# Kernel tuning notes

Measured on AMD Instinct MI355X. Metric: run time of the kernel, lower is better.

The kernel has to match this reference:

```python
import jax, jax.numpy as jnp
import numpy as np

B, S, E, H = 4, 2048, 2048, 1  # batch, seq, n_embd, n_head (source only runs with H=1)
LN_EPS = 1e-5


def _layernorm(x, g, b):
    m = jnp.mean(x, axis=-1, keepdims=True)
    v = jnp.mean(jnp.square(x - m), axis=-1, keepdims=True)
    return (x - m) * jax.lax.rsqrt(v + LN_EPS) * g + b


def setup_inputs() -> dict:
    key = jax.random.key(0)
    ks = jax.random.split(key, 8)
    sc = 0.02
    return {
        "x": jax.random.normal(ks[0], (B, S, E), jnp.float32),
        "mask": jnp.ones((B, S, 1, 1), jnp.int32),
        # attention params (torch Linear stored transposed: (in, out))
        "w_attn": jax.random.normal(ks[1], (E, H * E), jnp.float32) * sc,
        "b_attn": jnp.zeros((H * E,), jnp.float32),
        "w_kv": jax.random.normal(ks[2], (E, H * E), jnp.float32) * sc,
        "b_kv": jnp.zeros((H * E,), jnp.float32),
        "ln1_g": jnp.ones((E,), jnp.float32),
        "ln1_b": jnp.zeros((E,), jnp.float32),
        # MLP params
        "w_fc": jax.random.normal(ks[3], (E, 4 * E), jnp.float32) * sc,
        "b_fc": jnp.zeros((4 * E,), jnp.float32),
        "w_mproj": jax.random.normal(ks[4], (4 * E, E), jnp.float32) * sc,
        "b_mproj": jnp.zeros((E,), jnp.float32),
        "ln2_g": jnp.ones((E,), jnp.float32),
        "ln2_b": jnp.zeros((E,), jnp.float32),
    }


def reference(x, mask, w_attn, b_attn, w_kv, b_kv, ln1_g, ln1_b,
              w_fc, b_fc, w_mproj, b_mproj, ln2_g, ln2_b):
    # ---- Attention (faithful to source: einsum binds 'h' to the seq axis) ----
    h_attn = (x @ w_attn + b_attn).reshape(B, S, H, E)  # (b, s, h, d)
    h_proj = (x @ w_kv + b_kv).reshape(B, S, H, E)      # (b, s, h, d)
    # score[b, s, m, l] = sum_d h_attn[b, s, l, d] * h_proj[b, s, m, d]
    attn_score = jnp.einsum('bhld,bhmd->bhml', h_attn, h_proj)  # (B, S, H, H)
    attn_score = jnp.where(mask == 0, jnp.float32(-1e9), attn_score)
    attn_prob = jax.nn.softmax(attn_score, axis=-1)
    attn_vec = jnp.einsum('bhml,bhmd->bhld', attn_prob, h_proj)  # (B, S, H, E)
    attn_out = attn_vec.reshape(B, S, H * E)
    # (dropouts are identity in eval mode)
    # ---- Residual + LN + MLP + Residual + LN ----
    h = _layernorm(x + attn_out, ln1_g, ln1_b)
    h_mlp = jax.nn.gelu(h @ w_fc + b_fc, approximate=False)
    h_mlp = h_mlp @ w_mproj + b_mproj
    return _layernorm(h_mlp + x, ln2_g, ln2_b)
```

## Files before the change

kernel.cpp:

```cpp
#include <hip/hip_runtime.h>
#include <hip/hip_bf16.h>
#include <stdint.h>


typedef __attribute__((ext_vector_type(4))) float f32x4;
typedef __attribute__((ext_vector_type(8))) __bf16 bf16x8;
typedef __attribute__((ext_vector_type(8))) unsigned short ushort8;

__device__ __forceinline__ unsigned short f2bf(float f) {
  unsigned int u = __float_as_uint(f);
  return (unsigned short)((u + 0x7FFFu + ((u >> 16) & 1u)) >> 16);
}

__device__ __forceinline__ void gload_lds16(const void* g, void* l) {
  __builtin_amdgcn_global_load_lds(
      (const __attribute__((address_space(1))) unsigned int*)(uintptr_t)g,
      (__attribute__((address_space(3))) unsigned int*)(unsigned int)(uintptr_t)l,
      16, 0, 0);
}

#define WAITLGK(n) asm volatile("s_waitcnt lgkmcnt(" #n ")" ::: "memory")
#define WAITVM(n) asm volatile("s_waitcnt vmcnt(" #n ")" ::: "memory")
#define SBAR() __builtin_amdgcn_s_barrier()
#define SCHED0() __builtin_amdgcn_sched_barrier(0)

__global__ __launch_bounds__(256) void cvt_bf16_kernel(
    const float* __restrict__ in, unsigned short* __restrict__ out, int n8) {
  int i = blockIdx.x * 256 + threadIdx.x;
  if (i >= n8) return;
  const size_t base = (size_t)i * 8;
  float4 a = *(const float4*)(in + base);
  float4 b = *(const float4*)(in + base + 4);
  ushort8 o;
  o[0] = f2bf(a.x); o[1] = f2bf(a.y); o[2] = f2bf(a.z); o[3] = f2bf(a.w);
  o[4] = f2bf(b.x); o[5] = f2bf(b.y); o[6] = f2bf(b.z); o[7] = f2bf(b.w);
  *(ushort8*)(out + base) = o;
}

__global__ __launch_bounds__(256) void transpose_cvt(
    const float* __restrict__ W, unsigned short* __restrict__ WT, int R, int C) {
  __shared__ unsigned short t[64][66];
  const int c0 = blockIdx.x * 64, r0 = blockIdx.y * 64;
  const int tid = threadIdx.x;
  const int lr = tid >> 4;
  const int lc = (tid & 15) * 4;
#pragma unroll
  for (int p = 0; p < 4; ++p) {
    const int r = lr + p * 16;
    float4 v = *(const float4*)(W + (size_t)(r0 + r) * C + c0 + lc);
    t[r][lc + 0] = f2bf(v.x);
    t[r][lc + 1] = f2bf(v.y);
    t[r][lc + 2] = f2bf(v.z);
    t[r][lc + 3] = f2bf(v.w);
  }
  __syncthreads();
#pragma unroll
  for (int p = 0; p < 4; ++p) {
    const int oc = lr + p * 16;
    ushort4 o;
    o.x = t[lc + 0][oc];
    o.y = t[lc + 1][oc];
    o.z = t[lc + 2][oc];
    o.w = t[lc + 3][oc];
    *(ushort4*)(WT + (size_t)(c0 + oc) * R + r0 + lc) = o;
  }
}

template <int EPI>
__global__ __launch_bounds__(512, 2) void gemm256(
    const unsigned short* __restrict__ A, const unsigned short* __restrict__ BT,
    const float* __restrict__ bias, const float* __restrict__ xres,
    void* __restrict__ out, int N, int K) {
  __shared__ unsigned short lds[2][2][256 * 64];

  const int tid = threadIdx.x;
  const int lane = tid & 63;
  const int w = tid >> 6;
  const int wm = w >> 2;
  const int wn = w & 3;

  const int nbn = N / 256;
  const int nwg = gridDim.x;
  const int bid = blockIdx.x;
  const int wg = (bid & 7) * (nwg >> 3) + (bid >> 3);
  const int bm = wg / nbn, bn = wg % nbn;

  const int nt = K / 64;

  const int srow = w * 8 + (lane >> 3);
  const int schunk = (lane & 7) ^ ((lane >> 3) & 7);
  const unsigned short* gA = A + (size_t)(bm * 256 + srow) * K + schunk * 8;
  const unsigned short* gB = BT + (size_t)(bn * 256 + srow) * K + schunk * 8;

  auto STAGE = [&](int buf, int op, int half, int tile) {
    const int tc = tile < nt ? tile : nt - 1;
    const unsigned short* g =
        (op ? gB : gA) + (size_t)(half * 128) * K + (size_t)tc * 64;
    unsigned short* l = &lds[buf][op][(half * 128 + w * 8) * 64];
    gload_lds16(g, l);
    gload_lds16(g + (size_t)64 * K, l + 64 * 64);
  };

  const int rA = wm * 128 + (lane & 15);
  const int rB = wn * 64 + (lane & 15);
  const int kq = lane >> 4;
  const int x7 = lane & 7;
  const int c0 = ((kq ^ x7) << 4);
  const int c1 = (((4 + kq) ^ x7) << 4);

  f32x4 acc[8][4] = {};
  bf16x8 aS0[4][2], aS1[4][2], b0v[2][2], b1v[2][2];

#define READ_ALO(buf)                                              \
  {                                                                \
    const char* p = (const char*)&lds[buf][0][0] + rA * 128;       \
    _Pragma("unroll") for (int mf = 0; mf < 4; ++mf) {             \
      aS0[mf][0] = *(const bf16x8*)(p + mf * 2048 + c0);           \
      aS0[mf][1] = *(const bf16x8*)(p + mf * 2048 + c1);           \
    }                                                              \
  }
#define READ_AHI(buf)                                              \
  {                                                                \
    const char* p = (const char*)&lds[buf][0][0] + rA * 128 + 8192;\
    _Pragma("unroll") for (int mf = 0; mf < 4; ++mf) {             \
      aS1[mf][0] = *(const bf16x8*)(p + mf * 2048 + c0);           \
      aS1[mf][1] = *(const bf16x8*)(p + mf * 2048 + c1);           \
    }                                                              \
  }
#define READ_B0(buf)                                               \
  {                                                                \
    const char* p = (const char*)&lds[buf][1][0] + rB * 128;       \
    _Pragma("unroll") for (int nf = 0; nf < 2; ++nf) {             \
      b0v[nf][0] = *(const bf16x8*)(p + nf * 2048 + c0);           \
      b0v[nf][1] = *(const bf16x8*)(p + nf * 2048 + c1);           \
    }                                                              \
  }
#define READ_B1(buf)                                               \
  {                                                                \
    const char* p = (const char*)&lds[buf][1][0] + rB * 128 + 4096;\
    _Pragma("unroll") for (int nf = 0; nf < 2; ++nf) {             \
      b1v[nf][0] = *(const bf16x8*)(p + nf * 2048 + c0);           \
      b1v[nf][1] = *(const bf16x8*)(p + nf * 2048 + c1);           \
    }                                                              \
  }
#define CLUSTER(ASET, BSET, MO, NO)                                         \
  __builtin_amdgcn_s_setprio(1);                                            \
  _Pragma("unroll") for (int mf = 0; mf < 4; ++mf)                          \
      _Pragma("unroll") for (int nf = 0; nf < 2; ++nf)                      \
          _Pragma("unroll") for (int ks = 0; ks < 2; ++ks)                  \
              acc[MO + mf][NO + nf] =                                       \
                  __builtin_amdgcn_mfma_f32_16x16x32_bf16(                  \
                      ASET[mf][ks], BSET[nf][ks], acc[MO + mf][NO + nf],    \
                      0, 0, 0);                                             \
  __builtin_amdgcn_s_setprio(0);

  STAGE(0, 0, 0, 0); STAGE(0, 0, 1, 0); STAGE(0, 1, 0, 0); STAGE(0, 1, 1, 0);
  STAGE(1, 0, 0, 1); STAGE(1, 0, 1, 1); STAGE(1, 1, 0, 1); STAGE(1, 1, 1, 1);
  WAITVM(8);
  SBAR();
  READ_ALO(0);
  READ_B0(0);

  for (int t = 0; t < nt; ++t) {
    const int cb = t & 1, ob = cb ^ 1;
    READ_B1(cb);
    WAITLGK(4);
    SCHED0();
    CLUSTER(aS0, b0v, 0, 0);
    SBAR();
    READ_AHI(cb);
    WAITLGK(8);
    SCHED0();
    CLUSTER(aS0, b1v, 0, 2);
    SBAR();
    STAGE(cb, 0, 0, t + 2);
    WAITLGK(0);
    SCHED0();
    CLUSTER(aS1, b0v, 4, 0);
    WAITVM(2);
    SBAR();
    READ_ALO(ob);
    READ_B0(ob);
    STAGE(cb, 0, 1, t + 2);
    STAGE(cb, 1, 0, t + 2);
    STAGE(cb, 1, 1, t + 2);
    WAITLGK(12);
    SCHED0();
    CLUSTER(aS1, b1v, 4, 2);
    SBAR();
  }
  WAITVM(0);

  const int col0 = bn * 256 + wn * 64 + (lane & 15);
  const int row0 = bm * 256 + wm * 128 + ((lane >> 4) << 2);
  float bv[4];
#pragma unroll
  for (int n = 0; n < 4; ++n) bv[n] = bias[col0 + n * 16];
#pragma unroll
  for (int mf = 0; mf < 8; ++mf) {
#pragma unroll
    for (int j = 0; j < 4; ++j) {
      const size_t row = (size_t)(row0 + mf * 16 + j);
#pragma unroll
      for (int n = 0; n < 4; ++n) {
        const size_t idx = row * N + col0 + n * 16;
        float v = acc[mf][n][j] + bv[n];
        if (EPI == 0) {
          ((float*)out)[idx] = v + xres[idx];
        } else {
          float ge = 0.5f * v * (1.0f + erff(v * 0.7071067811865475f));
          ((unsigned short*)out)[idx] = f2bf(ge);
        }
      }
    }
  }
#undef READ_ALO
#undef READ_AHI
#undef READ_B0
#undef READ_B1
#undef CLUSTER
}

template <int OUT_BF16>
__global__ __launch_bounds__(256) void ln_row(const float* __restrict__ tin,
                                              const float* __restrict__ gw,
                                              const float* __restrict__ bw,
                                              void* __restrict__ outp) {
  const int row = blockIdx.x;
  const int tid = threadIdx.x;
  const size_t base = (size_t)row * 2048 + tid * 8;
  alignas(16) float v[8];
  *(float4*)(v) = *(const float4*)(tin + base);
  *(float4*)(v + 4) = *(const float4*)(tin + base + 4);
  float s = 0.f, q = 0.f;
#pragma unroll
  for (int i = 0; i < 8; ++i) { s += v[i]; q += v[i] * v[i]; }
#pragma unroll
  for (int m = 32; m >= 1; m >>= 1) {
    s += __shfl_xor(s, m);
    q += __shfl_xor(q, m);
  }
  __shared__ float red[8];
  if ((tid & 63) == 0) {
    red[tid >> 6] = s;
    red[4 + (tid >> 6)] = q;
  }
  __syncthreads();
  s = red[0] + red[1] + red[2] + red[3];
  q = red[4] + red[5] + red[6] + red[7];
  const float mean = s * (1.0f / 2048.0f);
  float var = q * (1.0f / 2048.0f) - mean * mean;
  var = fmaxf(var, 0.0f);
  const float rstd = rsqrtf(var + 1e-5f);
  alignas(16) float gv[8], bv[8];
  *(float4*)(gv) = *(const float4*)(gw + (size_t)tid * 8);
  *(float4*)(gv + 4) = *(const float4*)(gw + (size_t)tid * 8 + 4);
  *(float4*)(bv) = *(const float4*)(bw + (size_t)tid * 8);
  *(float4*)(bv + 4) = *(const float4*)(bw + (size_t)tid * 8 + 4);
  if (OUT_BF16) {
    ushort8 o;
#pragma unroll
    for (int i = 0; i < 8; ++i)
      o[i] = f2bf((v[i] - mean) * rstd * gv[i] + bv[i]);
    *(ushort8*)((unsigned short*)outp + base) = o;
  } else {
    alignas(16) float r[8];
#pragma unroll
    for (int i = 0; i < 8; ++i) r[i] = (v[i] - mean) * rstd * gv[i] + bv[i];
    *(float4*)((float*)outp + base) = *(float4*)(r);
    *(float4*)((float*)outp + base + 4) = *(float4*)(r + 4);
  }
}

extern "C" void kernel_launch(void* const* d_in, const int* in_sizes, int n_in,
                              void* d_out, int out_size, void* d_ws,
                              size_t ws_size, hipStream_t stream) {
  constexpr int M = 8192;
  constexpr int E = 2048;
  constexpr int F = 8192;
  const size_t MiB = 1ull << 20;

  const float* x = (const float*)d_in[0];
  const float* w_kv = (const float*)d_in[4];
  const float* b_kv = (const float*)d_in[5];
  const float* ln1_g = (const float*)d_in[6];
  const float* ln1_b = (const float*)d_in[7];
  const float* w_fc = (const float*)d_in[8];
  const float* b_fc = (const float*)d_in[9];
  const float* w_mproj = (const float*)d_in[10];
  const float* b_mproj = (const float*)d_in[11];
  const float* ln2_g = (const float*)d_in[12];
  const float* ln2_b = (const float*)d_in[13];
  float* out = (float*)d_out;
  char* ws = (char*)d_ws;

  float* tbuf = out;

  int nch;
  unsigned short *xb, *wkvT, *wfcT, *wmpT, *hb, *gch;
  if (ws_size >= 224 * MiB) {
    nch = 1;
    gch = (unsigned short*)(ws + 0);
    xb = (unsigned short*)(ws + 0);
    wkvT = (unsigned short*)(ws + 32 * MiB);
    wfcT = (unsigned short*)(ws + 128 * MiB);
    wmpT = (unsigned short*)(ws + 160 * MiB);
    hb = (unsigned short*)(ws + 192 * MiB);
  } else if (ws_size >= 160 * MiB) {
    nch = 2;
    gch = (unsigned short*)(ws + 0);
    xb = (unsigned short*)(ws + 0);
    wkvT = (unsigned short*)(ws + 32 * MiB);
    hb = (unsigned short*)(ws + 64 * MiB);
    wfcT = (unsigned short*)(ws + 96 * MiB);
    wmpT = (unsigned short*)(ws + 128 * MiB);
  } else {
    nch = 4;
    gch = (unsigned short*)(ws + 0);
    xb = (unsigned short*)(ws + 0);
    wkvT = (unsigned short*)(ws + 32 * MiB);
    hb = (unsigned short*)(ws + 32 * MiB);
    wfcT = (unsigned short*)(ws + 64 * MiB);
    wmpT = (unsigned short*)(ws + 96 * MiB);
  }

  cvt_bf16_kernel<<<(M * E / 8 + 255) / 256, 256, 0, stream>>>(x, xb, M * E / 8);
  transpose_cvt<<<dim3(E / 64, E / 64), 256, 0, stream>>>(w_kv, wkvT, E, E);
  transpose_cvt<<<dim3(F / 64, E / 64), 256, 0, stream>>>(w_fc, wfcT, E, F);
  transpose_cvt<<<dim3(E / 64, F / 64), 256, 0, stream>>>(w_mproj, wmpT, F, E);

  gemm256<0><<<(M / 256) * (E / 256), 512, 0, stream>>>(xb, wkvT, b_kv, x,
                                                        tbuf, E, E);
  ln_row<1><<<M, 256, 0, stream>>>(tbuf, ln1_g, ln1_b, hb);
  const int Mc = M / nch;
  for (int c = 0; c < nch; ++c) {
    const size_t roff = (size_t)c * Mc;
    gemm256<1><<<(Mc / 256) * (F / 256), 512, 0, stream>>>(
        hb + roff * E, wfcT, b_fc, nullptr, gch, F, E);
    gemm256<0><<<(Mc / 256) * (E / 256), 512, 0, stream>>>(
        gch, wmpT, b_mproj, x + roff * E, tbuf + roff * E, E, F);
  }
  ln_row<0><<<M, 256, 0, stream>>>(tbuf, ln2_g, ln2_b, out);
}
```

Measured before the change: 689.7 us.

## Restructure GEMM LDS layout into quarter tiles with finer-grained 8-wave staging schedule

Reorganizes the GEMM shared-memory buffer into per-half sub-tiles so each staged chunk matches one MFMA cluster's operands. The main loop is unrolled by two tiles, and global-to-LDS loads are interleaved at quarter granularity between MFMA clusters with explicit vmcnt/lgkmcnt waits and barriers. Only one A fragment set stays in registers, which lowers register pressure. The aim is to overlap loads with compute more evenly, at the cost of more barriers per tile and a riskier hand-written dependency schedule.

```diff
diff --git a/kernel.cpp b/kernel.cpp
--- a/kernel.cpp
+++ b/kernel.cpp
@@ -22,7 +22,6 @@
 #define WAITLGK(n) asm volatile("s_waitcnt lgkmcnt(" #n ")" ::: "memory")
 #define WAITVM(n) asm volatile("s_waitcnt vmcnt(" #n ")" ::: "memory")
 #define SBAR() __builtin_amdgcn_s_barrier()
-#define SCHED0() __builtin_amdgcn_sched_barrier(0)
 
 __global__ __launch_bounds__(256) void cvt_bf16_kernel(
     const float* __restrict__ in, unsigned short* __restrict__ out, int n8) {
@@ -71,13 +70,14 @@
     const unsigned short* __restrict__ A, const unsigned short* __restrict__ BT,
     const float* __restrict__ bias, const float* __restrict__ xres,
     void* __restrict__ out, int N, int K) {
-  __shared__ unsigned short lds[2][2][256 * 64];
+  __shared__ unsigned short L[2][2][2][8192];
 
   const int tid = threadIdx.x;
   const int lane = tid & 63;
   const int w = tid >> 6;
   const int wm = w >> 2;
   const int wn = w & 3;
+  const int l15 = lane & 15;
 
   const int nbn = N / 256;
   const int nwg = gridDim.x;
@@ -89,109 +89,123 @@
 
   const int srow = w * 8 + (lane >> 3);
   const int schunk = (lane & 7) ^ ((lane >> 3) & 7);
-  const unsigned short* gA = A + (size_t)(bm * 256 + srow) * K + schunk * 8;
-  const unsigned short* gB = BT + (size_t)(bn * 256 + srow) * K + schunk * 8;
-
-  auto STAGE = [&](int buf, int op, int half, int tile) {
-    const int tc = tile < nt ? tile : nt - 1;
-    const unsigned short* g =
-        (op ? gB : gA) + (size_t)(half * 128) * K + (size_t)tc * 64;
-    unsigned short* l = &lds[buf][op][(half * 128 + w * 8) * 64];
-    gload_lds16(g, l);
-    gload_lds16(g + (size_t)64 * K, l + 64 * 64);
-  };
-
-  const int rA = wm * 128 + (lane & 15);
-  const int rB = wn * 64 + (lane & 15);
+  const unsigned short* pb[2][2][2];
+#pragma unroll
+  for (int h = 0; h < 2; ++h)
+#pragma unroll
+    for (int j = 0; j < 2; ++j) {
+      pb[0][h][j] =
+          A + (size_t)(bm * 256 + j * 128 + h * 64 + srow) * K + schunk * 8;
+      pb[1][h][j] = BT +
+                    (size_t)(bn * 256 + ((srow >> 5) + 2 * j) * 64 + h * 32 +
+                             (srow & 31)) * K +
+                    schunk * 8;
+    }
+
+#define STAGE(BUF, OP, H, TILE)                                            \
+  {                                                                        \
+    const size_t ko_ = (size_t)(TILE) * 64;                                \
+    gload_lds16(pb[OP][H][0] + ko_, &L[BUF][OP][H][w * 512]);              \
+    gload_lds16(pb[OP][H][1] + ko_, &L[BUF][OP][H][w * 512 + 4096]);       \
+  }
+
   const int kq = lane >> 4;
   const int x7 = lane & 7;
-  const int c0 = ((kq ^ x7) << 4);
-  const int c1 = (((4 + kq) ^ x7) << 4);
+  const int cc0 = ((kq ^ x7) << 4);
+  const int cc1 = (((4 + kq) ^ x7) << 4);
+  const int rAoff = (wm * 64 + l15) * 128;
+  const int rBoff = (wn * 32 + l15) * 128;
 
   f32x4 acc[8][4] = {};
-  bf16x8 aS0[4][2], aS1[4][2], b0v[2][2], b1v[2][2];
-
-#define READ_ALO(buf)                                              \
-  {                                                                \
-    const char* p = (const char*)&lds[buf][0][0] + rA * 128;       \
-    _Pragma("unroll") for (int mf = 0; mf < 4; ++mf) {             \
-      aS0[mf][0] = *(const bf16x8*)(p + mf * 2048 + c0);           \
-      aS0[mf][1] = *(const bf16x8*)(p + mf * 2048 + c1);           \
-    }                                                              \
-  }
-#define READ_AHI(buf)                                              \
-  {                                                                \
-    const char* p = (const char*)&lds[buf][0][0] + rA * 128 + 8192;\
-    _Pragma("unroll") for (int mf = 0; mf < 4; ++mf) {             \
-      aS1[mf][0] = *(const bf16x8*)(p + mf * 2048 + c0);           \
-      aS1[mf][1] = *(const bf16x8*)(p + mf * 2048 + c1);           \
-    }                                                              \
-  }
-#define READ_B0(buf)                                               \
-  {                                                                \
-    const char* p = (const char*)&lds[buf][1][0] + rB * 128;       \
-    _Pragma("unroll") for (int nf = 0; nf < 2; ++nf) {             \
-      b0v[nf][0] = *(const bf16x8*)(p + nf * 2048 + c0);           \
-      b0v[nf][1] = *(const bf16x8*)(p + nf * 2048 + c1);           \
-    }                                                              \
-  }
-#define READ_B1(buf)                                               \
-  {                                                                \
-    const char* p = (const char*)&lds[buf][1][0] + rB * 128 + 4096;\
-    _Pragma("unroll") for (int nf = 0; nf < 2; ++nf) {             \
-      b1v[nf][0] = *(const bf16x8*)(p + nf * 2048 + c0);           \
-      b1v[nf][1] = *(const bf16x8*)(p + nf * 2048 + c1);           \
-    }                                                              \
-  }
-#define CLUSTER(ASET, BSET, MO, NO)                                         \
+  bf16x8 aF[4][2], b0F[2][2], b1F[2][2];
+
+#define RD_A(BUF, H)                                                   \
+  {                                                                    \
+    const char* p_ = (const char*)&L[BUF][0][H][0] + rAoff;            \
+    _Pragma("unroll") for (int mf = 0; mf < 4; ++mf) {                 \
+      aF[mf][0] = *(const bf16x8*)(p_ + mf * 2048 + cc0);              \
+      aF[mf][1] = *(const bf16x8*)(p_ + mf * 2048 + cc1);              \
+    }                                                                  \
+  }
+#define RD_B(BUF, H, DST)                                              \
+  {                                                                    \
+    const char* p_ = (const char*)&L[BUF][1][H][0] + rBoff;            \
+    _Pragma("unroll") for (int nf = 0; nf < 2; ++nf) {                 \
+      DST[nf][0] = *(const bf16x8*)(p_ + nf * 2048 + cc0);             \
+      DST[nf][1] = *(const bf16x8*)(p_ + nf * 2048 + cc1);             \
+    }                                                                  \
+  }
+#define CLUSTER(BSET, MO, NO)                                               \
   __builtin_amdgcn_s_setprio(1);                                            \
   _Pragma("unroll") for (int mf = 0; mf < 4; ++mf)                          \
       _Pragma("unroll") for (int nf = 0; nf < 2; ++nf)                      \
           _Pragma("unroll") for (int ks = 0; ks < 2; ++ks)                  \
               acc[MO + mf][NO + nf] =                                       \
                   __builtin_amdgcn_mfma_f32_16x16x32_bf16(                  \
-                      ASET[mf][ks], BSET[nf][ks], acc[MO + mf][NO + nf],    \
+                      aF[mf][ks], BSET[nf][ks], acc[MO + mf][NO + nf],      \
                       0, 0, 0);                                             \
   __builtin_amdgcn_s_setprio(0);
 
-  STAGE(0, 0, 0, 0); STAGE(0, 0, 1, 0); STAGE(0, 1, 0, 0); STAGE(0, 1, 1, 0);
-  STAGE(1, 0, 0, 1); STAGE(1, 0, 1, 1); STAGE(1, 1, 0, 1); STAGE(1, 1, 1, 1);
+  STAGE(0, 0, 0, 0);
+  STAGE(0, 1, 0, 0);
+  STAGE(0, 0, 1, 0);
+  STAGE(0, 1, 1, 0);
+  STAGE(1, 0, 0, 1);
+  STAGE(1, 1, 0, 1);
   WAITVM(8);
   SBAR();
-  READ_ALO(0);
-  READ_B0(0);
-
-  for (int t = 0; t < nt; ++t) {
-    const int cb = t & 1, ob = cb ^ 1;
-    READ_B1(cb);
-    WAITLGK(4);
-    SCHED0();
-    CLUSTER(aS0, b0v, 0, 0);
-    SBAR();
-    READ_AHI(cb);
+
+  for (int t2 = 0; t2 < nt; t2 += 2) {
+    const int tn2 = (t2 + 2 < nt) ? t2 + 2 : nt - 1;
+    const int tn3 = (t2 + 3 < nt) ? t2 + 3 : nt - 1;
+    RD_A(0, 0); RD_B(0, 0, b0F);
+    STAGE(1, 0, 1, t2 + 1);
     WAITLGK(8);
-    SCHED0();
-    CLUSTER(aS0, b1v, 0, 2);
-    SBAR();
-    STAGE(cb, 0, 0, t + 2);
-    WAITLGK(0);
-    SCHED0();
-    CLUSTER(aS1, b0v, 4, 0);
-    WAITVM(2);
-    SBAR();
-    READ_ALO(ob);
-    READ_B0(ob);
-    STAGE(cb, 0, 1, t + 2);
-    STAGE(cb, 1, 0, t + 2);
-    STAGE(cb, 1, 1, t + 2);
-    WAITLGK(12);
-    SCHED0();
-    CLUSTER(aS1, b1v, 4, 2);
+    SBAR(); WAITLGK(0);
+    CLUSTER(b0F, 0, 0);
+    WAITVM(6);
+    SBAR();
+    RD_B(0, 1, b1F);
+    STAGE(1, 1, 1, t2 + 1);
+    SBAR(); WAITLGK(0);
+    CLUSTER(b1F, 0, 2);
+    SBAR();
+    RD_A(0, 1);
+    STAGE(0, 0, 0, tn2);
+    SBAR(); WAITLGK(0);
+    CLUSTER(b0F, 4, 0);
+    SBAR();
+    STAGE(0, 1, 0, tn2);
+    SBAR();
+    CLUSTER(b1F, 4, 2);
+    WAITVM(8);
+    SBAR();
+    RD_A(1, 0); RD_B(1, 0, b0F);
+    STAGE(0, 0, 1, tn2);
+    WAITLGK(8);
+    SBAR(); WAITLGK(0);
+    CLUSTER(b0F, 0, 0);
+    WAITVM(6);
+    SBAR();
+    RD_B(1, 1, b1F);
+    STAGE(0, 1, 1, tn2);
+    SBAR(); WAITLGK(0);
+    CLUSTER(b1F, 0, 2);
+    SBAR();
+    RD_A(1, 1);
+    STAGE(1, 0, 0, tn3);
+    SBAR(); WAITLGK(0);
+    CLUSTER(b0F, 4, 0);
+    SBAR();
+    STAGE(1, 1, 0, tn3);
+    SBAR();
+    CLUSTER(b1F, 4, 2);
+    WAITVM(8);
     SBAR();
   }
   WAITVM(0);
 
-  const int col0 = bn * 256 + wn * 64 + (lane & 15);
+  const int col0 = bn * 256 + wn * 64 + l15;
   const int row0 = bm * 256 + wm * 128 + ((lane >> 4) << 2);
   float bv[4];
 #pragma unroll
@@ -214,11 +228,10 @@
       }
     }
   }
-#undef READ_ALO
-#undef READ_AHI
-#undef READ_B0
-#undef READ_B1
+#undef RD_A
+#undef RD_B
 #undef CLUSTER
+#undef STAGE
 }
 
 template <int OUT_BF16>
```

Result: no change. 686.8 us (-0.4%).
